# Kernel optimization log

Measured on AMD Instinct MI355X. Metric: run time of the kernel, lower is better.

## Reference

```python
import jax, jax.numpy as jnp
import numpy as np

EPS = 1e-5

def conv1d(x, w, b, pad):
    # x: [N, Cin, T], w: [Cout, Cin, K]
    y = jax.lax.conv_general_dilated(x, w, (1,), [(pad, pad)],
                                     dimension_numbers=("NCH", "OIH", "NCH"))
    return y + b[None, :, None]

def bn_eval(x, gamma, beta, mean, var):
    # BatchNorm1d in inference mode over channel dim of [N, C, T]
    inv = gamma / jnp.sqrt(var + EPS)
    return x * inv[None, :, None] + (beta - mean * inv)[None, :, None]

def setup_inputs() -> dict:
    key = jax.random.key(0)
    ks = jax.random.split(key, 16)
    B, E, N, T = 8, 16, 64, 128
    D, OUT = 32, 64  # timeseries_dim, output_dim
    inp = {
        "node_features": jax.random.normal(ks[0], (B, E, N, T, 1), dtype=jnp.float32),
        "edge_features": jax.random.normal(ks[1], (B, E, T), dtype=jnp.float32),
        "conv1_w": jax.random.normal(ks[2], (D, 1, 3), dtype=jnp.float32) * 0.3,
        "conv1_b": jax.random.normal(ks[3], (D,), dtype=jnp.float32) * 0.1,
        "conv2_w": jax.random.normal(ks[4], (1, D, 3), dtype=jnp.float32) * 0.1,
        "conv2_b": jax.random.normal(ks[5], (1,), dtype=jnp.float32) * 0.1,
        "conv3_w": jax.random.normal(ks[6], (OUT, 1, 1), dtype=jnp.float32) * 0.3,
        "conv3_b": jax.random.normal(ks[7], (OUT,), dtype=jnp.float32) * 0.1,
        "bn1_gamma": jax.random.uniform(ks[8], (D,), dtype=jnp.float32) + 0.5,
        "bn1_beta": jax.random.normal(ks[9], (D,), dtype=jnp.float32) * 0.1,
        "bn1_mean": jax.random.normal(ks[10], (D,), dtype=jnp.float32) * 0.1,
        "bn1_var": jax.random.uniform(ks[11], (D,), dtype=jnp.float32) + 0.5,
        "bn2_gamma": jax.random.uniform(ks[12], (1,), dtype=jnp.float32) + 0.5,
        "bn2_beta": jax.random.normal(ks[13], (1,), dtype=jnp.float32) * 0.1,
        "bn2_mean": jax.random.normal(ks[14], (1,), dtype=jnp.float32) * 0.1,
        "bn2_var": jax.random.uniform(ks[15], (1,), dtype=jnp.float32) + 0.5,
    }
    return inp

def reference(node_features, edge_features, conv1_w, conv1_b, conv2_w, conv2_b,
              conv3_w, conv3_b, bn1_gamma, bn1_beta, bn1_mean, bn1_var,
              bn2_gamma, bn2_beta, bn2_mean, bn2_var):
    B, E, N, T, _ = node_features.shape
    OUT = conv3_w.shape[0]
    # Self-connectivity: each (b,e,n) node processes its own [1,1,T] series and
    # the sum over its (single) connected edge is the identity. Fuse the triple
    # python loop into one batched conv pipeline over B*E*N series.
    x = node_features.reshape(B * E * N, 1, T)          # [BEN, 1, T]
    x = jax.nn.relu(bn_eval(conv1d(x, conv1_w, conv1_b, 1),
                            bn1_gamma, bn1_beta, bn1_mean, bn1_var))  # [BEN, D, T]
    x = jax.nn.relu(bn_eval(conv1d(x, conv2_w, conv2_b, 1),
                            bn2_gamma, bn2_beta, bn2_mean, bn2_var))  # [BEN, 1, T]
    x = conv1d(x, conv3_w, conv3_b, 0)                  # [BEN, OUT, T]
    return x.reshape(B, E, N, OUT, T)
```

## Files before the change

### kernel.cpp

```cpp
#include <hip/hip_runtime.h>

#define EPSF 1e-5f

typedef float f32x4 __attribute__((ext_vector_type(4)));


__global__ __launch_bounds__(128) void hnc_kernel(
    const float* __restrict__ x_in,
    const float* __restrict__ w1,
    const float* __restrict__ b1,
    const float* __restrict__ w2,
    const float* __restrict__ b2,
    const float* __restrict__ w3,
    const float* __restrict__ b3,
    const float* __restrict__ g1, const float* __restrict__ be1,
    const float* __restrict__ m1, const float* __restrict__ v1,
    const float* __restrict__ g2, const float* __restrict__ be2,
    const float* __restrict__ m2, const float* __restrict__ v2,
    float* __restrict__ out)
{
    const int T = 128, OUT = 64;

    __shared__ float x_s[132];
    __shared__ float y2_s[128];
    __shared__ float a1_s[3][32];
    __shared__ float c1_s[32];
    __shared__ float w2f_s[3][32];
    __shared__ float w3_s[64];
    __shared__ float b3_s[64];
    __shared__ float c2_s;

    const int tid = threadIdx.x;
    const int series = blockIdx.x;

    x_s[2 + tid] = x_in[(size_t)series * T + tid];
    if (tid < 2) x_s[tid] = 0.f;
    else if (tid < 4) x_s[128 + tid] = 0.f;

    if (tid < 32) {
        float inv = g1[tid] * rsqrtf(v1[tid] + EPSF);
        a1_s[0][tid] = inv * w1[tid * 3 + 0];
        a1_s[1][tid] = inv * w1[tid * 3 + 1];
        a1_s[2][tid] = inv * w1[tid * 3 + 2];
        c1_s[tid] = b1[tid] * inv + be1[tid] - m1[tid] * inv;
    } else if (tid < 64) {
        int d = tid - 32;
        float s2 = g2[0] * rsqrtf(v2[0] + EPSF);
        w2f_s[0][d] = s2 * w2[d * 3 + 0];
        w2f_s[1][d] = s2 * w2[d * 3 + 1];
        w2f_s[2][d] = s2 * w2[d * 3 + 2];
        if (d == 0) c2_s = b2[0] * s2 + be2[0] - m2[0] * s2;
    } else if (tid < 128) {
        int o = tid - 64;
        w3_s[o] = w3[o];
        b3_s[o] = b3[o];
    }
    __syncthreads();

    const float xm2 = x_s[tid];
    const float xm1 = x_s[tid + 1];
    const float x0  = x_s[tid + 2];
    const float xp1 = x_s[tid + 3];
    const float xp2 = x_s[tid + 4];

    float accm = 0.f, acc0 = 0.f, accp = 0.f;
    #pragma unroll 4
    for (int d = 0; d < 32; ++d) {
        const float a0 = a1_s[0][d], a1 = a1_s[1][d], a2 = a1_s[2][d];
        const float c  = c1_s[d];
        float ym = fmaxf(fmaf(a0, xm2, fmaf(a1, xm1, fmaf(a2, x0,  c))), 0.f);
        float y0 = fmaxf(fmaf(a0, xm1, fmaf(a1, x0,  fmaf(a2, xp1, c))), 0.f);
        float yp = fmaxf(fmaf(a0, x0,  fmaf(a1, xp1, fmaf(a2, xp2, c))), 0.f);
        accm = fmaf(w2f_s[0][d], ym, accm);
        acc0 = fmaf(w2f_s[1][d], y0, acc0);
        accp = fmaf(w2f_s[2][d], yp, accp);
    }
    const float mm = (tid == 0)   ? 0.f : 1.f;
    const float mp = (tid == 127) ? 0.f : 1.f;
    y2_s[tid] = fmaxf(fmaf(mm, accm, fmaf(mp, accp, acc0 + c2_s)), 0.f);
    __syncthreads();

    f32x4* out4 = (f32x4*)(out + (size_t)series * OUT * T);
    #pragma unroll
    for (int i = 0; i < 16; ++i) {
        int flat4 = i * 128 + tid;
        int o = flat4 >> 5;
        int t = (flat4 << 2) & 127;
        f32x4 y = *(const f32x4*)&y2_s[t];
        float w = w3_s[o], b = b3_s[o];
        f32x4 r;
        r.x = fmaf(w, y.x, b);
        r.y = fmaf(w, y.y, b);
        r.z = fmaf(w, y.z, b);
        r.w = fmaf(w, y.w, b);
        out4[flat4] = r;
    }
}

extern "C" void kernel_launch(void* const* d_in, const int* in_sizes, int n_in,
                              void* d_out, int out_size, void* d_ws, size_t ws_size,
                              hipStream_t stream) {
    const float* x   = (const float*)d_in[0];
    const float* w1  = (const float*)d_in[2];
    const float* b1  = (const float*)d_in[3];
    const float* w2  = (const float*)d_in[4];
    const float* b2  = (const float*)d_in[5];
    const float* w3  = (const float*)d_in[6];
    const float* b3  = (const float*)d_in[7];
    const float* g1  = (const float*)d_in[8];
    const float* be1 = (const float*)d_in[9];
    const float* m1  = (const float*)d_in[10];
    const float* v1  = (const float*)d_in[11];
    const float* g2  = (const float*)d_in[12];
    const float* be2 = (const float*)d_in[13];
    const float* m2  = (const float*)d_in[14];
    const float* v2  = (const float*)d_in[15];

    const int T = 128;
    const int n_series = in_sizes[0] / T;

    hnc_kernel<<<n_series, 128, 0, stream>>>(x, w1, b1, w2, b2, w3, b3,
                                             g1, be1, m1, v1, g2, be2, m2, v2,
                                             (float*)d_out);
}
```

Baseline: 51.93 us.

## Process four series per block with double-buffered input prefetch and packed weights

Each block now handles four consecutive series instead of one. This spreads the per-block weight folding and launch setup across more work, and the next series' input is prefetched into a second shared buffer while the current one is computed and written. Conv1 and conv2 weights are packed into float4 shared arrays so one vector LDS read replaces several scalar reads, and the y2 vector is loaded once per thread instead of once per output row. The cost is a quarter as many blocks (8192 instead of 32768), which lowers parallelism and latency hiding for an output-write-bound kernel. It also assumes the series count is divisible by four.

```diff
diff --git a/kernel.cpp b/kernel.cpp
--- a/kernel.cpp
+++ b/kernel.cpp
@@ -1,6 +1,7 @@
 #include <hip/hip_runtime.h>
 
 #define EPSF 1e-5f
+#define SER 4
 
 typedef float f32x4 __attribute__((ext_vector_type(4)));
 
@@ -19,81 +20,97 @@
     const float* __restrict__ m2, const float* __restrict__ v2,
     float* __restrict__ out)
 {
-    const int T = 128, OUT = 64;
-
-    __shared__ float x_s[132];
-    __shared__ float y2_s[128];
-    __shared__ float a1_s[3][32];
-    __shared__ float c1_s[32];
-    __shared__ float w2f_s[3][32];
+    __shared__ float x_s[2][132];
+    __shared__ float y2_s[2][128];
+    __shared__ f32x4 pkA_s[32];
+    __shared__ f32x4 pkB_s[32];
     __shared__ float w3_s[64];
     __shared__ float b3_s[64];
     __shared__ float c2_s;
 
     const int tid = threadIdx.x;
-    const int series = blockIdx.x;
+    const size_t s0 = (size_t)blockIdx.x * SER;
 
-    x_s[2 + tid] = x_in[(size_t)series * T + tid];
-    if (tid < 2) x_s[tid] = 0.f;
-    else if (tid < 4) x_s[128 + tid] = 0.f;
+    x_s[0][2 + tid] = x_in[s0 * 128 + tid];
+    if (tid < 2)      { x_s[0][tid] = 0.f;       x_s[1][tid] = 0.f; }
+    else if (tid < 4) { x_s[0][128 + tid] = 0.f; x_s[1][128 + tid] = 0.f; }
 
     if (tid < 32) {
-        float inv = g1[tid] * rsqrtf(v1[tid] + EPSF);
-        a1_s[0][tid] = inv * w1[tid * 3 + 0];
-        a1_s[1][tid] = inv * w1[tid * 3 + 1];
-        a1_s[2][tid] = inv * w1[tid * 3 + 2];
-        c1_s[tid] = b1[tid] * inv + be1[tid] - m1[tid] * inv;
+        const int d = tid;
+        float inv = g1[d] * rsqrtf(v1[d] + EPSF);
+        f32x4 A;
+        A.x = inv * w1[d * 3 + 0];
+        A.y = inv * w1[d * 3 + 1];
+        A.z = inv * w1[d * 3 + 2];
+        A.w = b1[d] * inv + be1[d] - m1[d] * inv;
+        pkA_s[d] = A;
     } else if (tid < 64) {
-        int d = tid - 32;
+        const int d = tid - 32;
         float s2 = g2[0] * rsqrtf(v2[0] + EPSF);
-        w2f_s[0][d] = s2 * w2[d * 3 + 0];
-        w2f_s[1][d] = s2 * w2[d * 3 + 1];
-        w2f_s[2][d] = s2 * w2[d * 3 + 2];
+        f32x4 W;
+        W.x = s2 * w2[d * 3 + 0];
+        W.y = s2 * w2[d * 3 + 1];
+        W.z = s2 * w2[d * 3 + 2];
+        W.w = 0.f;
+        pkB_s[d] = W;
         if (d == 0) c2_s = b2[0] * s2 + be2[0] - m2[0] * s2;
-    } else if (tid < 128) {
-        int o = tid - 64;
+    } else {
+        const int o = tid - 64;
         w3_s[o] = w3[o];
         b3_s[o] = b3[o];
     }
     __syncthreads();
 
-    const float xm2 = x_s[tid];
-    const float xm1 = x_s[tid + 1];
-    const float x0  = x_s[tid + 2];
-    const float xp1 = x_s[tid + 3];
-    const float xp2 = x_s[tid + 4];
-
-    float accm = 0.f, acc0 = 0.f, accp = 0.f;
-    #pragma unroll 4
-    for (int d = 0; d < 32; ++d) {
-        const float a0 = a1_s[0][d], a1 = a1_s[1][d], a2 = a1_s[2][d];
-        const float c  = c1_s[d];
-        float ym = fmaxf(fmaf(a0, xm2, fmaf(a1, xm1, fmaf(a2, x0,  c))), 0.f);
-        float y0 = fmaxf(fmaf(a0, xm1, fmaf(a1, x0,  fmaf(a2, xp1, c))), 0.f);
-        float yp = fmaxf(fmaf(a0, x0,  fmaf(a1, xp1, fmaf(a2, xp2, c))), 0.f);
-        accm = fmaf(w2f_s[0][d], ym, accm);
-        acc0 = fmaf(w2f_s[1][d], y0, acc0);
-        accp = fmaf(w2f_s[2][d], yp, accp);
-    }
     const float mm = (tid == 0)   ? 0.f : 1.f;
     const float mp = (tid == 127) ? 0.f : 1.f;
-    y2_s[tid] = fmaxf(fmaf(mm, accm, fmaf(mp, accp, acc0 + c2_s)), 0.f);
-    __syncthreads();
+    const int   og = tid >> 5;
+    const int   ty = (tid << 2) & 127;
 
-    f32x4* out4 = (f32x4*)(out + (size_t)series * OUT * T);
-    #pragma unroll
-    for (int i = 0; i < 16; ++i) {
-        int flat4 = i * 128 + tid;
-        int o = flat4 >> 5;
-        int t = (flat4 << 2) & 127;
-        f32x4 y = *(const f32x4*)&y2_s[t];
-        float w = w3_s[o], b = b3_s[o];
-        f32x4 r;
-        r.x = fmaf(w, y.x, b);
-        r.y = fmaf(w, y.y, b);
-        r.z = fmaf(w, y.z, b);
-        r.w = fmaf(w, y.w, b);
-        out4[flat4] = r;
+    for (int s = 0; s < SER; ++s) {
+        const int cur = s & 1, nxt = cur ^ 1;
+
+        float xpre = 0.f;
+        if (s + 1 < SER) xpre = x_in[(s0 + s + 1) * 128 + tid];
+
+        const float xm2 = x_s[cur][tid];
+        const float xm1 = x_s[cur][tid + 1];
+        const float x0  = x_s[cur][tid + 2];
+        const float xp1 = x_s[cur][tid + 3];
+        const float xp2 = x_s[cur][tid + 4];
+
+        float accm = 0.f, acc0 = 0.f, accp = 0.f;
+        #pragma unroll 4
+        for (int d = 0; d < 32; ++d) {
+            const f32x4 A = pkA_s[d];
+            const f32x4 W = pkB_s[d];
+            float ym = fmaxf(fmaf(A.x, xm2, fmaf(A.y, xm1, fmaf(A.z, x0,  A.w))), 0.f);
+            float y0 = fmaxf(fmaf(A.x, xm1, fmaf(A.y, x0,  fmaf(A.z, xp1, A.w))), 0.f);
+            float yp = fmaxf(fmaf(A.x, x0,  fmaf(A.y, xp1, fmaf(A.z, xp2, A.w))), 0.f);
+            accm = fmaf(W.x, ym, accm);
+            acc0 = fmaf(W.y, y0, acc0);
+            accp = fmaf(W.z, yp, accp);
+        }
+        y2_s[cur][tid] = fmaxf(fmaf(mm, accm, fmaf(mp, accp, acc0 + c2_s)), 0.f);
+        __syncthreads();
+
+        const f32x4 y = *(const f32x4*)&y2_s[cur][ty];
+        f32x4* out4 = (f32x4*)(out + (s0 + s) * 64 * 128);
+        #pragma unroll
+        for (int i = 0; i < 16; ++i) {
+            const int o = 4 * i + og;
+            const float w = w3_s[o], b = b3_s[o];
+            f32x4 r;
+            r.x = fmaf(w, y.x, b);
+            r.y = fmaf(w, y.y, b);
+            r.z = fmaf(w, y.z, b);
+            r.w = fmaf(w, y.w, b);
+            out4[i * 128 + tid] = r;
+        }
+
+        if (s + 1 < SER) {
+            x_s[nxt][2 + tid] = xpre;
+            __syncthreads();
+        }
     }
 }
 
@@ -118,8 +135,9 @@
 
     const int T = 128;
     const int n_series = in_sizes[0] / T;
+    const int n_blocks = n_series / SER;
 
-    hnc_kernel<<<n_series, 128, 0, stream>>>(x, w1, b1, w2, b2, w3, b3,
+    hnc_kernel<<<n_blocks, 128, 0, stream>>>(x, w1, b1, w2, b2, w3, b3,
                                              g1, be1, m1, v1, g2, be2, m2, v2,
                                              (float*)d_out);
 }
```

New measurement: 50.83 us. 1.02x faster.
